# Performance work log

Hardware: AMD Instinct MI355X
Metric: run time of the kernel (lower is better)

## Reference

```python
import jax, jax.numpy as jnp
import numpy as np


def setup_inputs() -> dict:
    key = jax.random.key(0)
    kq, kk, kv = jax.random.split(key, 3)
    B, H, S, D = 2, 8, 4096, 64
    return {
        "query": jax.random.normal(kq, (B, H, S, D), dtype=jnp.float32),
        "key": jax.random.normal(kk, (B, H, S, D), dtype=jnp.float32),
        "value": jax.random.normal(kv, (B, H, S, D), dtype=jnp.float32),
    }


def reference(query, key, value):
    # NOTE: the torch source overwrites sqrt(d) with d, so the divisor is D, not sqrt(D).
    d = query.shape[-1]
    # score: [B, H, S_q, S_k]
    score = jnp.einsum("bhqd,bhkd->bhqk", query, key) / d
    relu = jax.nn.relu(score)  # no softmax / row normalization
    out = jnp.einsum("bhqk,bhkd->bhqd", relu, value)
    return out
```

## Files before the change

### kernel.cpp

```cpp
#include <hip/hip_runtime.h>
#include <hip/hip_bf16.h>
#include <stdint.h>


#define NH 16
#define SEQ 4096
#define DD 64
#define HE (SEQ*DD)
#define HB (HE*2)
#define Q16_OFF 0
#define K16_OFF (NH*HB)
#define V16_OFF (2*NH*HB)
#define WS_NEED (3*NH*HB)

typedef __attribute__((ext_vector_type(8)))  short    bf16x8;
typedef __attribute__((ext_vector_type(16))) float    f32x16;
typedef __attribute__((ext_vector_type(4)))  uint32_t u32x4;

__device__ inline uint32_t f2bf1(float f) {
  return (uint32_t)__builtin_bit_cast(unsigned short, __float2bfloat16(f));
}
__device__ inline uint32_t pack2bf(float a, float b) {
  return f2bf1(a) | (f2bf1(b) << 16);
}
__device__ inline uint32_t cvtpk(float lo, float hi) {
  uint32_t r;
  asm("v_cvt_pk_bf16_f32 %0, %1, %2" : "=v"(r) : "v"(lo), "v"(hi));
  return r;
}
__device__ inline uint32_t relu2(uint32_t w) {
  uint32_t r;
  asm("v_pk_max_f16 %0, %1, 0" : "=v"(r) : "v"(w));
  return r;
}

__global__ __launch_bounds__(256) void prepass_kernel(const float* __restrict__ Q,
                                                      const float* __restrict__ K,
                                                      const float* __restrict__ V,
                                                      char* __restrict__ ws) {
  __shared__ float vt[64*65];
  int bx = blockIdx.x, tid = threadIdx.x;
  if (bx < 2048) {
    int head = bx >> 7, qg = bx & 127;
    int r31 = tid & 31, c = tid >> 5;
    const float4* s = (const float4*)(Q + (size_t)head*HE + ((size_t)(qg*32 + r31))*64 + c*8);
    float4 a = s[0], b = s[1];
    const float sc = 1.0f/64.0f;
    u32x4 o;
    o.x = pack2bf(a.x*sc, a.y*sc);
    o.y = pack2bf(a.z*sc, a.w*sc);
    o.z = pack2bf(b.x*sc, b.y*sc);
    o.w = pack2bf(b.z*sc, b.w*sc);
    char* tb = ws + Q16_OFF + (size_t)head*HB;
    *(u32x4*)(tb + ((qg*4 + (c >> 1))*1024) + ((c & 1)*32 + r31)*16) = o;
  } else if (bx < 3072) {
    int tile = bx - 2048;
    int head = tile >> 6, t = tile & 63;
    int r = tid >> 2, c0 = (tid & 3) * 16;
    const float4* s4 = (const float4*)(K + (size_t)head*HE + ((size_t)(t*64 + r))*64 + c0);
    float4 f0 = s4[0], f1 = s4[1], f2 = s4[2], f3 = s4[3];
    u32x4 c_lo, c_hi;
    c_lo.x = pack2bf(f0.x, f0.y); c_lo.y = pack2bf(f0.z, f0.w);
    c_lo.z = pack2bf(f1.x, f1.y); c_lo.w = pack2bf(f1.z, f1.w);
    c_hi.x = pack2bf(f2.x, f2.y); c_hi.y = pack2bf(f2.z, f2.w);
    c_hi.z = pack2bf(f3.x, f3.y); c_hi.w = pack2bf(f3.z, f3.w);
    char* tb = ws + K16_OFF + ((size_t)head*64 + t)*8192;
    char* chunk = tb + ((r >> 5)*4 + (tid & 3))*1024 + (r & 31)*16;
    *(u32x4*)(chunk)       = c_lo;
    *(u32x4*)(chunk + 512) = c_hi;
  } else {
    int tile = bx - 3072;
    int head = tile >> 6, t = tile & 63;
    int k = tid >> 2, c0 = (tid & 3)*16;
    const float4* s4 = (const float4*)(V + (size_t)head*HE + ((size_t)(t*64 + k))*64 + c0);
    float4 f0 = s4[0], f1 = s4[1], f2 = s4[2], f3 = s4[3];
    float tmp[16] = {f0.x,f0.y,f0.z,f0.w, f1.x,f1.y,f1.z,f1.w,
                     f2.x,f2.y,f2.z,f2.w, f3.x,f3.y,f3.z,f3.w};
    #pragma unroll
    for (int j = 0; j < 16; ++j) vt[k*65 + c0 + j] = tmp[j];
    __syncthreads();
    int d = tid >> 2, k0 = (tid & 3)*16;
    float v2[16];
    #pragma unroll
    for (int j = 0; j < 16; ++j) v2[j] = vt[(k0 + j)*65 + d];
    u32x4 c_lo, c_hi;
    c_lo.x = pack2bf(v2[0],  v2[1]);  c_lo.y = pack2bf(v2[2],  v2[3]);
    c_lo.z = pack2bf(v2[4],  v2[5]);  c_lo.w = pack2bf(v2[6],  v2[7]);
    c_hi.x = pack2bf(v2[8],  v2[9]);  c_hi.y = pack2bf(v2[10], v2[11]);
    c_hi.z = pack2bf(v2[12], v2[13]); c_hi.w = pack2bf(v2[14], v2[15]);
    char* tb = ws + V16_OFF + ((size_t)head*64 + t)*8192;
    char* chunk = tb + ((d >> 5)*4 + (tid & 3))*1024 + (d & 31)*16;
    *(u32x4*)(chunk)       = c_lo;
    *(u32x4*)(chunk + 512) = c_hi;
  }
}

__global__ __launch_bounds__(256, 2) void attn_kernel(const char* __restrict__ ws,
                                                      float* __restrict__ out) {
  int bid = blockIdx.x;
  int bx = (bid & 7) * 64 + (bid >> 3);
  int head = bx >> 5, qblk = bx & 31;
  int tid = threadIdx.x;
  int lane = tid & 63, w = tid >> 6;
  int l31 = lane & 31, h = lane >> 5;

  const char* q16   = ws + Q16_OFF + (size_t)head*HB;
  const char* kbase = ws + K16_OFF + (size_t)head*HB;
  const char* vbase = ws + V16_OFF + (size_t)head*HB;

  int qg = qblk*4 + w;
  bf16x8 qf[4];
  #pragma unroll
  for (int t = 0; t < 4; ++t)
    qf[t] = *(const bf16x8*)(q16 + ((size_t)(qg*4 + t))*1024 + lane*16);

  f32x16 kZero;
  #pragma unroll
  for (int i = 0; i < 16; ++i) kZero[i] = 0.f;

  f32x16 o[2];
  #pragma unroll
  for (int nd = 0; nd < 2; ++nd)
    #pragma unroll
    for (int i = 0; i < 16; ++i) o[nd][i] = 0.f;

  bf16x8 kfA[2][4], kfB[2][4], vf[2][4];

  auto loadK = [&](bf16x8 (&kf)[2][4], int kt) {
    const char* kp = kbase + (size_t)kt*8192;
    #pragma unroll
    for (int i = 0; i < 8; ++i)
      kf[i >> 2][i & 3] = *(const bf16x8*)(kp + i*1024 + lane*16);
  };
  auto loadV = [&](int kt) {
    const char* vp = vbase + (size_t)kt*8192;
    #pragma unroll
    for (int i = 0; i < 8; ++i)
      vf[i >> 2][i & 3] = *(const bf16x8*)(vp + i*1024 + lane*16);
  };

  auto computeT = [&](bf16x8 (&kf)[2][4]) {
    f32x16 st[2];
    #pragma unroll
    for (int n = 0; n < 2; ++n) {
      __builtin_amdgcn_s_setprio(1);
      f32x16 acc = __builtin_amdgcn_mfma_f32_32x32x16_bf16(kf[n][0], qf[0], kZero, 0, 0, 0);
      #pragma unroll
      for (int t = 1; t < 4; ++t)
        acc = __builtin_amdgcn_mfma_f32_32x32x16_bf16(kf[n][t], qf[t], acc, 0, 0, 0);
      st[n] = acc;
      __builtin_amdgcn_s_setprio(0);
    }
    bf16x8 pa[4];
    #pragma unroll
    for (int n = 0; n < 2; ++n)
      #pragma unroll
      for (int kn = 0; kn < 2; ++kn) {
        uint32_t w0 = cvtpk(st[n][kn*8+0], st[n][kn*8+1]);
        uint32_t w1 = cvtpk(st[n][kn*8+2], st[n][kn*8+3]);
        uint32_t w2 = cvtpk(st[n][kn*8+4], st[n][kn*8+5]);
        uint32_t w3 = cvtpk(st[n][kn*8+6], st[n][kn*8+7]);
        asm("v_permlane32_swap_b32 %0, %1" : "+v"(w0), "+v"(w2));
        asm("v_permlane32_swap_b32 %0, %1" : "+v"(w1), "+v"(w3));
        union { uint32_t u[4]; bf16x8 v; } pk;
        pk.u[0] = relu2(w0);
        pk.u[1] = relu2(w1);
        pk.u[2] = relu2(w2);
        pk.u[3] = relu2(w3);
        pa[n*2 + kn] = pk.v;
      }
    __builtin_amdgcn_s_setprio(1);
    #pragma unroll
    for (int nd = 0; nd < 2; ++nd)
      #pragma unroll
      for (int ks = 0; ks < 4; ++ks)
        o[nd] = __builtin_amdgcn_mfma_f32_32x32x16_bf16(pa[ks], vf[nd][ks], o[nd], 0, 0, 0);
    __builtin_amdgcn_s_setprio(0);
  };

  loadK(kfA, 0);
  #pragma unroll 1
  for (int kt = 0; kt < 64; kt += 2) {
    loadV(kt);
    loadK(kfB, (kt + 1) & 63);
    computeT(kfA);
    loadV(kt + 1);
    loadK(kfA, (kt + 2) & 63);
    computeT(kfB);
    if ((kt & 7) == 6) __builtin_amdgcn_s_barrier();
  }

  float* outh = out + (size_t)head*HE;
  #pragma unroll
  for (int nd = 0; nd < 2; ++nd)
    #pragma unroll
    for (int r = 0; r < 16; ++r) {
      int ql = w*32 + (r & 3) + 8*(r >> 2) + 4*h;
      outh[(size_t)(qblk*128 + ql)*64 + nd*32 + l31] = o[nd][r];
    }
}

extern "C" void kernel_launch(void* const* d_in, const int* in_sizes, int n_in,
                              void* d_out, int out_size, void* d_ws, size_t ws_size,
                              hipStream_t stream) {
  if (n_in < 3 || ws_size < (size_t)WS_NEED) return;
  const float* Q = (const float*)d_in[0];
  const float* K = (const float*)d_in[1];
  const float* V = (const float*)d_in[2];
  float* out = (float*)d_out;
  char* ws = (char*)d_ws;
  hipLaunchKernelGGL(prepass_kernel, dim3(4096), dim3(256), 0, stream, Q, K, V, ws);
  hipLaunchKernelGGL(attn_kernel,    dim3(512),  dim3(256), 0, stream, ws, out);
}
```

Before: 89.84 us.

## Split key range across two wave groups with LDS reduction and software-pipelined PV

Doubles the block to 512 threads. Two groups of four waves each process half of the key tiles for the same query block, and their partial outputs are summed through shared memory before the store. The inner loop is also restructured so the bf16 pack and ReLU of the next tile's scores interleave with the PV MFMAs of the previous tile, which hides the conversion latency. This adds occupancy and latency hiding per CU, at the cost of a 32KB LDS reduction, an extra sync, and more register pressure.

```diff
diff --git a/kernel.cpp b/kernel.cpp
--- a/kernel.cpp
+++ b/kernel.cpp
@@ -95,20 +95,23 @@
   }
 }
 
-__global__ __launch_bounds__(256, 2) void attn_kernel(const char* __restrict__ ws,
+__global__ __launch_bounds__(512, 2) void attn_kernel(const char* __restrict__ ws,
                                                       float* __restrict__ out) {
+  __shared__ float red[128*64];
   int bid = blockIdx.x;
   int bx = (bid & 7) * 64 + (bid >> 3);
   int head = bx >> 5, qblk = bx & 31;
   int tid = threadIdx.x;
   int lane = tid & 63, w = tid >> 6;
   int l31 = lane & 31, h = lane >> 5;
+  int g  = w >> 2;
+  int wq = w & 3;
 
   const char* q16   = ws + Q16_OFF + (size_t)head*HB;
-  const char* kbase = ws + K16_OFF + (size_t)head*HB;
-  const char* vbase = ws + V16_OFF + (size_t)head*HB;
-
-  int qg = qblk*4 + w;
+  const char* kbase = ws + K16_OFF + (size_t)head*HB + (size_t)g*32*8192;
+  const char* vbase = ws + V16_OFF + (size_t)head*HB + (size_t)g*32*8192;
+
+  int qg = qblk*4 + wq;
   bf16x8 qf[4];
   #pragma unroll
   for (int t = 0; t < 4; ++t)
@@ -124,9 +127,10 @@
     #pragma unroll
     for (int i = 0; i < 16; ++i) o[nd][i] = 0.f;
 
-  bf16x8 kfA[2][4], kfB[2][4], vf[2][4];
-
-  auto loadK = [&](bf16x8 (&kf)[2][4], int kt) {
+  bf16x8 kf[2][4], vf[2][4], paA[4], paB[4];
+  f32x16 st[2];
+
+  auto loadK = [&](int kt) {
     const char* kp = kbase + (size_t)kt*8192;
     #pragma unroll
     for (int i = 0; i < 8; ++i)
@@ -138,66 +142,98 @@
     for (int i = 0; i < 8; ++i)
       vf[i >> 2][i & 3] = *(const bf16x8*)(vp + i*1024 + lane*16);
   };
-
-  auto computeT = [&](bf16x8 (&kf)[2][4]) {
-    f32x16 st[2];
-    #pragma unroll
-    for (int n = 0; n < 2; ++n) {
-      __builtin_amdgcn_s_setprio(1);
-      f32x16 acc = __builtin_amdgcn_mfma_f32_32x32x16_bf16(kf[n][0], qf[0], kZero, 0, 0, 0);
-      #pragma unroll
-      for (int t = 1; t < 4; ++t)
-        acc = __builtin_amdgcn_mfma_f32_32x32x16_bf16(kf[n][t], qf[t], acc, 0, 0, 0);
-      st[n] = acc;
-      __builtin_amdgcn_s_setprio(0);
+  auto qkt = [&]() {
+    __builtin_amdgcn_s_setprio(1);
+    st[0] = __builtin_amdgcn_mfma_f32_32x32x16_bf16(kf[0][0], qf[0], kZero, 0, 0, 0);
+    st[1] = __builtin_amdgcn_mfma_f32_32x32x16_bf16(kf[1][0], qf[0], kZero, 0, 0, 0);
+    #pragma unroll
+    for (int t = 1; t < 4; ++t) {
+      st[0] = __builtin_amdgcn_mfma_f32_32x32x16_bf16(kf[0][t], qf[t], st[0], 0, 0, 0);
+      st[1] = __builtin_amdgcn_mfma_f32_32x32x16_bf16(kf[1][t], qf[t], st[1], 0, 0, 0);
     }
-    bf16x8 pa[4];
-    #pragma unroll
-    for (int n = 0; n < 2; ++n)
-      #pragma unroll
-      for (int kn = 0; kn < 2; ++kn) {
-        uint32_t w0 = cvtpk(st[n][kn*8+0], st[n][kn*8+1]);
-        uint32_t w1 = cvtpk(st[n][kn*8+2], st[n][kn*8+3]);
-        uint32_t w2 = cvtpk(st[n][kn*8+4], st[n][kn*8+5]);
-        uint32_t w3 = cvtpk(st[n][kn*8+6], st[n][kn*8+7]);
-        asm("v_permlane32_swap_b32 %0, %1" : "+v"(w0), "+v"(w2));
-        asm("v_permlane32_swap_b32 %0, %1" : "+v"(w1), "+v"(w3));
-        union { uint32_t u[4]; bf16x8 v; } pk;
-        pk.u[0] = relu2(w0);
-        pk.u[1] = relu2(w1);
-        pk.u[2] = relu2(w2);
-        pk.u[3] = relu2(w3);
-        pa[n*2 + kn] = pk.v;
-      }
+    __builtin_amdgcn_s_setprio(0);
+  };
+  auto packg = [&](bf16x8* paDst, int n, int kn) {
+    uint32_t w0 = cvtpk(st[n][kn*8+0], st[n][kn*8+1]);
+    uint32_t w1 = cvtpk(st[n][kn*8+2], st[n][kn*8+3]);
+    uint32_t w2 = cvtpk(st[n][kn*8+4], st[n][kn*8+5]);
+    uint32_t w3 = cvtpk(st[n][kn*8+6], st[n][kn*8+7]);
+    asm("v_permlane32_swap_b32 %0, %1" : "+v"(w0), "+v"(w2));
+    asm("v_permlane32_swap_b32 %0, %1" : "+v"(w1), "+v"(w3));
+    union { uint32_t u[4]; bf16x8 v; } pk;
+    pk.u[0] = relu2(w0);
+    pk.u[1] = relu2(w1);
+    pk.u[2] = relu2(w2);
+    pk.u[3] = relu2(w3);
+    paDst[n*2 + kn] = pk.v;
+  };
+  auto pv_pack = [&](bf16x8* paSrc, bf16x8* paDst) {
     __builtin_amdgcn_s_setprio(1);
+    o[0] = __builtin_amdgcn_mfma_f32_32x32x16_bf16(paSrc[0], vf[0][0], o[0], 0, 0, 0);
+    o[1] = __builtin_amdgcn_mfma_f32_32x32x16_bf16(paSrc[0], vf[1][0], o[1], 0, 0, 0);
+    packg(paDst, 0, 0);
+    o[0] = __builtin_amdgcn_mfma_f32_32x32x16_bf16(paSrc[1], vf[0][1], o[0], 0, 0, 0);
+    o[1] = __builtin_amdgcn_mfma_f32_32x32x16_bf16(paSrc[1], vf[1][1], o[1], 0, 0, 0);
+    packg(paDst, 0, 1);
+    o[0] = __builtin_amdgcn_mfma_f32_32x32x16_bf16(paSrc[2], vf[0][2], o[0], 0, 0, 0);
+    o[1] = __builtin_amdgcn_mfma_f32_32x32x16_bf16(paSrc[2], vf[1][2], o[1], 0, 0, 0);
+    packg(paDst, 1, 0);
+    o[0] = __builtin_amdgcn_mfma_f32_32x32x16_bf16(paSrc[3], vf[0][3], o[0], 0, 0, 0);
+    o[1] = __builtin_amdgcn_mfma_f32_32x32x16_bf16(paSrc[3], vf[1][3], o[1], 0, 0, 0);
+    packg(paDst, 1, 1);
+    __builtin_amdgcn_s_setprio(0);
+  };
+
+  loadK(0);
+  loadV(0);
+  qkt();
+  loadK(1);
+  packg(paA, 0, 0); packg(paA, 0, 1); packg(paA, 1, 0); packg(paA, 1, 1);
+
+  #pragma unroll 1
+  for (int kt = 1; kt < 31; kt += 2) {
+    qkt();
+    loadK(kt + 1);
+    pv_pack(paA, paB);
+    loadV(kt);
+    qkt();
+    loadK(kt + 2);
+    pv_pack(paB, paA);
+    loadV(kt + 1);
+  }
+  qkt();
+  pv_pack(paA, paB);
+  loadV(31);
+  __builtin_amdgcn_s_setprio(1);
+  #pragma unroll
+  for (int ks = 0; ks < 4; ++ks) {
+    o[0] = __builtin_amdgcn_mfma_f32_32x32x16_bf16(paB[ks], vf[0][ks], o[0], 0, 0, 0);
+    o[1] = __builtin_amdgcn_mfma_f32_32x32x16_bf16(paB[ks], vf[1][ks], o[1], 0, 0, 0);
+  }
+  __builtin_amdgcn_s_setprio(0);
+
+  __syncthreads();
+  if (g == 1) {
     #pragma unroll
     for (int nd = 0; nd < 2; ++nd)
       #pragma unroll
-      for (int ks = 0; ks < 4; ++ks)
-        o[nd] = __builtin_amdgcn_mfma_f32_32x32x16_bf16(pa[ks], vf[nd][ks], o[nd], 0, 0, 0);
-    __builtin_amdgcn_s_setprio(0);
-  };
-
-  loadK(kfA, 0);
-  #pragma unroll 1
-  for (int kt = 0; kt < 64; kt += 2) {
-    loadV(kt);
-    loadK(kfB, (kt + 1) & 63);
-    computeT(kfA);
-    loadV(kt + 1);
-    loadK(kfA, (kt + 2) & 63);
-    computeT(kfB);
-    if ((kt & 7) == 6) __builtin_amdgcn_s_barrier();
-  }
-
-  float* outh = out + (size_t)head*HE;
-  #pragma unroll
-  for (int nd = 0; nd < 2; ++nd)
-    #pragma unroll
-    for (int r = 0; r < 16; ++r) {
-      int ql = w*32 + (r & 3) + 8*(r >> 2) + 4*h;
-      outh[(size_t)(qblk*128 + ql)*64 + nd*32 + l31] = o[nd][r];
-    }
+      for (int r = 0; r < 16; ++r) {
+        int ql = wq*32 + (r & 3) + 8*(r >> 2) + 4*h;
+        red[ql*64 + nd*32 + l31] = o[nd][r];
+      }
+  }
+  __syncthreads();
+  if (g == 0) {
+    float* outh = out + (size_t)head*HE;
+    #pragma unroll
+    for (int nd = 0; nd < 2; ++nd)
+      #pragma unroll
+      for (int r = 0; r < 16; ++r) {
+        int ql = wq*32 + (r & 3) + 8*(r >> 2) + 4*h;
+        float v = o[nd][r] + red[ql*64 + nd*32 + l31];
+        outh[(size_t)(qblk*128 + ql)*64 + nd*32 + l31] = v;
+      }
+  }
 }
 
 extern "C" void kernel_launch(void* const* d_in, const int* in_sizes, int n_in,
@@ -210,5 +246,5 @@
   float* out = (float*)d_out;
   char* ws = (char*)d_ws;
   hipLaunchKernelGGL(prepass_kernel, dim3(4096), dim3(256), 0, stream, Q, K, V, ws);
-  hipLaunchKernelGGL(attn_kernel,    dim3(512),  dim3(256), 0, stream, ws, out);
-}
+  hipLaunchKernelGGL(attn_kernel,    dim3(512),  dim3(512), 0, stream, ws, out);
+}
```

New measurement: 90.38 us. No clear change (+0.6%).
